# Kernel optimization log

Measured on AMD Instinct MI355X. Metric: run time of the kernel, lower is better.

## Reference

```python
import jax, jax.numpy as jnp
import numpy as np

T, B, N, DIN, H, DOUT = 20, 32, 100, 2, 128, 2
BN = B * N


def setup_inputs() -> dict:
    key = jax.random.key(0)
    ks = jax.random.split(key, 12)
    x = jax.random.normal(ks[0], (T, BN, DIN), jnp.float32)
    A = jax.random.randint(ks[1], (T, BN, BN), 0, 2, jnp.int32)
    mask = jax.random.randint(ks[2], (T, BN), 0, 2, jnp.int32).astype(bool)
    s_g = 1.0 / np.sqrt(DIN)
    s_h = 1.0 / np.sqrt(H)
    u = lambda k, shp, s: jax.random.uniform(k, shp, jnp.float32, -s, s)
    return {
        'x': x, 'A': A, 'mask': mask, 'num_nodes': N,
        'W_gcn': u(ks[3], (DIN, H), s_g), 'b_gcn': jnp.zeros((H,), jnp.float32),
        'W_ih': u(ks[4], (H, 3 * H), s_h), 'b_ih': u(ks[5], (3 * H,), s_h),
        'W_hh': u(ks[6], (H, 3 * H), s_h), 'b_hh': u(ks[7], (3 * H,), s_h),
        'W_fc': u(ks[8], (H, DOUT), s_h), 'b_fc': u(ks[9], (DOUT,), s_h),
    }


def reference(x, A, mask, num_nodes, W_gcn, b_gcn, W_ih, b_ih, W_hh, b_hh, W_fc, b_fc):
    BN_ = x.shape[1]
    B_ = BN_ // num_nodes

    def step(h, inp):
        feats, A_t, m_t = inp
        mf = m_t.astype(jnp.float32)
        # masked subgraph adjacency + self loops only on masked nodes (PyG add_self_loops on subgraph)
        Ahat = A_t.astype(jnp.float32) * mf[:, None] * mf[None, :] + jnp.diag(mf)
        deg = Ahat.sum(axis=0)  # PyG gcn_norm: in-degree at edge_index[1] (column sum)
        dinv = jnp.where(deg > 0, jax.lax.rsqrt(deg), 0.0)
        xw = feats @ W_gcn  # [BN, H]
        # out[i] = dinv[i] * sum_j Ahat[j,i] * dinv[j] * xw[j]
        agg = dinv[:, None] * (Ahat.T @ (xw * dinv[:, None]))
        g = jax.nn.relu(agg + b_gcn)
        # torch GRUCell
        gi = g @ W_ih + b_ih
        gh = h @ W_hh + b_hh
        ir, iz, ig = jnp.split(gi, 3, axis=-1)
        hr, hz, hg = jnp.split(gh, 3, axis=-1)
        r = jax.nn.sigmoid(ir + hr)
        z = jax.nn.sigmoid(iz + hz)
        n = jnp.tanh(ig + r * hg)
        h_new = (1.0 - z) * n + z * h
        h = jnp.where(m_t[:, None], h_new, h)  # scatter-back: only masked nodes update
        return h, h

    h0 = jnp.zeros((BN_, H), jnp.float32)
    _, seq = jax.lax.scan(step, h0, (x, A, mask))  # [T, BN, H]
    seq = seq.reshape(x.shape[0], B_, num_nodes, H)
    out = seq @ W_fc + b_fc  # [T, B, N, DOUT]
    return out.transpose(1, 2, 0, 3)  # [B, N, T, DOUT]
```

## Files before the change

### kernel.cpp

```cpp
#include <hip/hip_runtime.h>
#include <math.h>

#define T_  20
#define BN  3200
#define H   128
#define N3H 384
#define DOUT 2
#define JW  400

typedef unsigned char u8;

__device__ __forceinline__ bool getm(const u8* m8, const int* m32, int fl, int idx) {
    return fl ? (m8[idx] != 0) : (m32[idx] != 0);
}

__global__ __launch_bounds__(256) void k_compact(const u8* __restrict__ m8,
                                                 const int* __restrict__ m32,
                                                 int* __restrict__ flag,
                                                 int* __restrict__ act_idx,
                                                 int* __restrict__ act_cnt) {
    int t = blockIdx.x, tid = threadIdx.x;
    __shared__ int lf;
    if (tid == 0) lf = 0;
    __syncthreads();
    bool hit = false;
    for (int j = tid; j < BN; j += 256) {
        if ((j & 3) && m8[t * BN + j]) hit = true;
    }
    if (__any(hit) && (tid & 63) == 0) atomicOr(&lf, 1);
    __syncthreads();
    int fl = lf;
    if (tid == 0 && fl) atomicOr(flag, 1);
    for (int j = tid; j < BN; j += 256) {
        if (getm(m8, m32, fl, t * BN + j)) {
            int pos = atomicAdd(&act_cnt[t], 1);
            act_idx[t * BN + pos] = j;
        }
    }
}

#define RCH 256
__global__ __launch_bounds__(256) void k_deg_pack(const int* __restrict__ A,
                                                  const int* __restrict__ act_idx,
                                                  const int* __restrict__ act_cnt,
                                                  u8* __restrict__ A1,
                                                  int* __restrict__ deg) {
    int t = blockIdx.z;
    int nact = act_cnt[t];
    int start = blockIdx.y * RCH;
    if (start >= nact) return;
    int n = min(RCH, nact - start);
    __shared__ int ai_s[RCH];
    int tid = threadIdx.x;
    if (tid < n) ai_s[tid] = act_idx[t * BN + start + tid];
    __syncthreads();

    int c = (blockIdx.x * 256 + tid) * 4;
    if (c >= BN) return;
    const int* At = A + (size_t)t * BN * BN;
    u8* A1t = A1 + ((size_t)t * JW + (start >> 3)) * BN + c;
    int cnt0 = 0, cnt1 = 0, cnt2 = 0, cnt3 = 0;
    int n8 = n & ~7;
    int jb = 0;
    for (; jb < n8; jb += 8) {
        unsigned b0 = 0, b1 = 0, b2 = 0, b3 = 0;
        #pragma unroll
        for (int q = 0; q < 8; ++q) {
            int j = ai_s[jb + q];
            int4 aa = *(const int4*)(At + (size_t)j * BN + c);
            cnt0 += aa.x; b0 |= (unsigned)aa.x << q;
            cnt1 += aa.y; b1 |= (unsigned)aa.y << q;
            cnt2 += aa.z; b2 |= (unsigned)aa.z << q;
            cnt3 += aa.w; b3 |= (unsigned)aa.w << q;
        }
        uchar4 pk; pk.x = (u8)b0; pk.y = (u8)b1; pk.z = (u8)b2; pk.w = (u8)b3;
        *(uchar4*)(A1t + (size_t)(jb >> 3) * BN) = pk;
    }
    if (jb < n) {
        unsigned b0 = 0, b1 = 0, b2 = 0, b3 = 0;
        for (int q = 0; q < n - jb; ++q) {
            int j = ai_s[jb + q];
            int4 aa = *(const int4*)(At + (size_t)j * BN + c);
            cnt0 += aa.x; b0 |= (unsigned)aa.x << q;
            cnt1 += aa.y; b1 |= (unsigned)aa.y << q;
            cnt2 += aa.z; b2 |= (unsigned)aa.z << q;
            cnt3 += aa.w; b3 |= (unsigned)aa.w << q;
        }
        uchar4 pk; pk.x = (u8)b0; pk.y = (u8)b1; pk.z = (u8)b2; pk.w = (u8)b3;
        *(uchar4*)(A1t + (size_t)(jb >> 3) * BN) = pk;
    }
    atomicAdd(&deg[t * BN + c], cnt0);
    atomicAdd(&deg[t * BN + c + 1], cnt1);
    atomicAdd(&deg[t * BN + c + 2], cnt2);
    atomicAdd(&deg[t * BN + c + 3], cnt3);
}

__global__ __launch_bounds__(256) void k_dinv_u(const int* __restrict__ deg,
                                                const u8* __restrict__ m8,
                                                const int* __restrict__ m32,
                                                const int* __restrict__ flag,
                                                const float* __restrict__ x,
                                                const int* __restrict__ act_idx,
                                                const int* __restrict__ act_cnt,
                                                float* __restrict__ dinv,
                                                float* __restrict__ u0c,
                                                float* __restrict__ u1c) {
    int idx = blockIdx.x * 256 + threadIdx.x;
    int fl = *flag;
    int t = idx / BN, r = idx - t * BN;
    dinv[idx] = getm(m8, m32, fl, idx) ? rsqrtf((float)(deg[idx] + 1)) : 0.f;
    float v0 = 0.f, v1 = 0.f;
    if (r < act_cnt[t]) {
        int j = act_idx[idx];
        float d = rsqrtf((float)(deg[t * BN + j] + 1));
        v0 = d * x[(size_t)(t * BN + j) * 2];
        v1 = d * x[(size_t)(t * BN + j) * 2 + 1];
    }
    u0c[idx] = v0;
    u1c[idx] = v1;
}

#define JSL 25
__global__ __launch_bounds__(256) void k_c(const u8* __restrict__ A1,
                                           const int* __restrict__ act_cnt,
                                           const float* __restrict__ u0c,
                                           const float* __restrict__ u1c,
                                           float* __restrict__ c0g,
                                           float* __restrict__ c1g) {
    int t = blockIdx.z, js = blockIdx.y;
    int c = blockIdx.x * 1024 + threadIdx.x * 4;
    if (c >= BN) return;
    int nactp = (act_cnt[t] + 7) >> 3;
    int jw0 = js * JSL, jw1 = min(jw0 + JSL, nactp);
    if (jw0 >= jw1) return;
    const u8* base = A1 + (size_t)t * JW * BN;
    const float* U0 = u0c + t * BN;
    const float* U1 = u1c + t * BN;
    float s0[4] = {0.f, 0.f, 0.f, 0.f}, s1[4] = {0.f, 0.f, 0.f, 0.f};
    for (int jw = jw0; jw < jw1; ++jw) {
        uchar4 aa = *(const uchar4*)(base + (size_t)jw * BN + c);
        unsigned bb[4] = {aa.x, aa.y, aa.z, aa.w};
        const float* Up0 = U0 + jw * 8;
        const float* Up1 = U1 + jw * 8;
        #pragma unroll
        for (int jb = 0; jb < 8; ++jb) {
            float w0 = Up0[jb], w1 = Up1[jb];
            #pragma unroll
            for (int k = 0; k < 4; ++k) {
                if ((bb[k] >> jb) & 1) { s0[k] += w0; s1[k] += w1; }
            }
        }
    }
    #pragma unroll
    for (int k = 0; k < 4; ++k) {
        atomicAdd(&c0g[t * BN + c + k], s0[k]);
        atomicAdd(&c1g[t * BN + c + k], s1[k]);
    }
}

__global__ __launch_bounds__(384) void k_gi(const float* __restrict__ dinv,
                                            const float* __restrict__ c0g,
                                            const float* __restrict__ c1g,
                                            const float* __restrict__ x,
                                            const float* __restrict__ Wg,
                                            const float* __restrict__ bg,
                                            const int* __restrict__ act_idx,
                                            const int* __restrict__ act_cnt,
                                            const float* __restrict__ Wih,
                                            const float* __restrict__ bih,
                                            float* __restrict__ GI) {
    int t = blockIdx.y;
    int nact = act_cnt[t];
    int sb = blockIdx.x * 32;
    if (sb >= nact) return;
    int ns = min(32, nact - sb);
    __shared__ float gs[32][H];
    __shared__ float e0s[32], e1s[32];
    __shared__ int ar[32];
    int tid = threadIdx.x;
    if (tid < 32) {
        int row = 0; float e0 = 0.f, e1 = 0.f;
        if (tid < ns) {
            row = act_idx[t * BN + sb + tid];
            int gi = t * BN + row;
            float d = dinv[gi];
            e0 = d * (c0g[gi] + d * x[(size_t)gi * 2]);
            e1 = d * (c1g[gi] + d * x[(size_t)gi * 2 + 1]);
        }
        ar[tid] = row; e0s[tid] = e0; e1s[tid] = e1;
    }
    __syncthreads();
    for (int u2 = tid; u2 < 32 * H; u2 += 384) {
        int r = u2 >> 7, h = u2 & 127;
        gs[r][h] = fmaxf(e0s[r] * Wg[h] + e1s[r] * Wg[H + h] + bg[h], 0.f);
    }
    __syncthreads();

    float acc[32];
    #pragma unroll
    for (int r = 0; r < 32; ++r) acc[r] = 0.f;
    for (int k = 0; k < H; k += 4) {
        float w0 = Wih[(size_t)k * N3H + tid];
        float w1 = Wih[(size_t)(k + 1) * N3H + tid];
        float w2 = Wih[(size_t)(k + 2) * N3H + tid];
        float w3 = Wih[(size_t)(k + 3) * N3H + tid];
        #pragma unroll
        for (int r = 0; r < 32; ++r) {
            float4 g4 = *(const float4*)&gs[r][k];
            acc[r] += g4.x * w0 + g4.y * w1 + g4.z * w2 + g4.w * w3;
        }
    }
    float bb = bih[tid];
    #pragma unroll
    for (int r = 0; r < 32; ++r) {
        if (r < ns)
            GI[((size_t)t * BN + ar[r]) * N3H + tid] = acc[r] + bb;
    }
}

__global__ __launch_bounds__(384) void k_gru(const float* __restrict__ GI,
                                             const float* __restrict__ Whh,
                                             const float* __restrict__ bhh,
                                             const u8* __restrict__ m8,
                                             const int* __restrict__ m32,
                                             const int* __restrict__ flag,
                                             const float* __restrict__ Wfc,
                                             const float* __restrict__ bfc,
                                             float* __restrict__ out) {
    int row0 = blockIdx.x * 16;
    int tid = threadIdx.x;
    int fl = *flag;
    __shared__ float hs[16][H];
    __shared__ float ghs[16][N3H];
    __shared__ float bhs[N3H];
    __shared__ int ms[16];
    for (int i = tid; i < 16 * H; i += 384) (&hs[0][0])[i] = 0.f;
    if (tid < N3H) bhs[tid] = bhh[tid];
    int lane = tid & 63, wv = tid >> 6;
    float wfa0 = Wfc[lane * 2],        wfa1 = Wfc[lane * 2 + 1];
    float wfb0 = Wfc[(lane + 64) * 2], wfb1 = Wfc[(lane + 64) * 2 + 1];
    float bf0 = bfc[0], bf1 = bfc[1];

    for (int t = 0; t < T_; ++t) {
        if (tid < 16) ms[tid] = getm(m8, m32, fl, t * BN + row0 + tid) ? 1 : 0;
        __syncthreads();
        int mrl[16];
        #pragma unroll
        for (int r = 0; r < 16; ++r) mrl[r] = ms[r];

        float pir[6], piz[6], pig[6];
        #pragma unroll
        for (int ii = 0; ii < 6; ++ii) {
            pir[ii] = 0.f; piz[ii] = 0.f; pig[ii] = 0.f;
            int i5 = tid + ii * 384;
            if (i5 < 16 * H) {
                int r = i5 >> 7, u = i5 & 127;
                if (ms[r]) {
                    size_t gb = ((size_t)t * BN + row0 + r) * N3H;
                    pir[ii] = GI[gb + u];
                    piz[ii] = GI[gb + 128 + u];
                    pig[ii] = GI[gb + 256 + u];
                }
            }
        }

        float acc[16];
        #pragma unroll
        for (int r = 0; r < 16; ++r) acc[r] = 0.f;
        for (int k = 0; k < H; k += 4) {
            float w0 = Whh[(size_t)k * N3H + tid];
            float w1 = Whh[(size_t)(k + 1) * N3H + tid];
            float w2 = Whh[(size_t)(k + 2) * N3H + tid];
            float w3 = Whh[(size_t)(k + 3) * N3H + tid];
            #pragma unroll
            for (int r = 0; r < 16; ++r) {
                if (mrl[r]) {
                    float4 h4 = *(const float4*)&hs[r][k];
                    acc[r] += h4.x * w0 + h4.y * w1 + h4.z * w2 + h4.w * w3;
                }
            }
        }
        #pragma unroll
        for (int r = 0; r < 16; ++r) ghs[r][tid] = acc[r];
        __syncthreads();

        #pragma unroll
        for (int ii = 0; ii < 6; ++ii) {
            int i5 = tid + ii * 384;
            if (i5 < 16 * H) {
                int r = i5 >> 7, u = i5 & 127;
                if (ms[r]) {
                    float hr = ghs[r][u] + bhs[u];
                    float hz = ghs[r][128 + u] + bhs[128 + u];
                    float hg = ghs[r][256 + u] + bhs[256 + u];
                    float rg = 1.f / (1.f + expf(-(pir[ii] + hr)));
                    float zg = 1.f / (1.f + expf(-(piz[ii] + hz)));
                    float ng = tanhf(pig[ii] + rg * hg);
                    hs[r][u] = (1.f - zg) * ng + zg * hs[r][u];
                }
            }
        }
        __syncthreads();

        for (int r = wv; r < 16; r += 6) {
            float h0 = hs[r][lane], h1 = hs[r][lane + 64];
            float p0 = h0 * wfa0 + h1 * wfb0;
            float p1 = h0 * wfa1 + h1 * wfb1;
            for (int o = 32; o > 0; o >>= 1) { p0 += __shfl_down(p0, o); p1 += __shfl_down(p1, o); }
            if (lane == 0) {
                out[((size_t)(row0 + r) * T_ + t) * DOUT]     = p0 + bf0;
                out[((size_t)(row0 + r) * T_ + t) * DOUT + 1] = p1 + bf1;
            }
        }
        __syncthreads();
    }
}

extern "C" void kernel_launch(void* const* d_in, const int* in_sizes, int n_in,
                              void* d_out, int out_size, void* d_ws, size_t ws_size,
                              hipStream_t stream) {
    const float* x    = (const float*)d_in[0];
    const int*   A    = (const int*)d_in[1];
    const u8*    m8   = (const u8*)d_in[2];
    const int*   m32  = (const int*)d_in[2];
    const float* Wg   = (const float*)d_in[4];
    const float* bg   = (const float*)d_in[5];
    const float* Wih  = (const float*)d_in[6];
    const float* bih  = (const float*)d_in[7];
    const float* Whh  = (const float*)d_in[8];
    const float* bhh  = (const float*)d_in[9];
    const float* Wfc  = (const float*)d_in[10];
    const float* bfc  = (const float*)d_in[11];
    float* out = (float*)d_out;

    char* ws = (char*)d_ws;
    size_t off = 0;
    auto alloc = [&](size_t bytes) {
        void* p = ws + off;
        off += (bytes + 255) & ~(size_t)255;
        return p;
    };
    int*   flag    = (int*)alloc(4);
    int*   act_cnt = (int*)alloc(T_ * 4);
    int*   deg     = (int*)alloc((size_t)T_ * BN * 4);
    float* c0g     = (float*)alloc((size_t)T_ * BN * 4);
    float* c1g     = (float*)alloc((size_t)T_ * BN * 4);
    size_t zbytes = off;
    int*   act_idx = (int*)alloc((size_t)T_ * BN * 4);
    float* dinv    = (float*)alloc((size_t)T_ * BN * 4);
    float* u0c     = (float*)alloc((size_t)T_ * BN * 4);
    float* u1c     = (float*)alloc((size_t)T_ * BN * 4);
    u8*    A1      = (u8*)alloc((size_t)T_ * JW * BN);
    float* GI      = (float*)alloc((size_t)T_ * BN * N3H * 4);

    hipMemsetAsync(ws, 0, zbytes, stream);
    k_compact<<<T_, 256, 0, stream>>>(m8, m32, flag, act_idx, act_cnt);
    k_deg_pack<<<dim3(4, 13, T_), 256, 0, stream>>>(A, act_idx, act_cnt, A1, deg);
    k_dinv_u<<<(T_ * BN) / 256, 256, 0, stream>>>(deg, m8, m32, flag, x, act_idx, act_cnt, dinv, u0c, u1c);
    k_c<<<dim3(4, 16, T_), 256, 0, stream>>>(A1, act_cnt, u0c, u1c, c0g, c1g);
    k_gi<<<dim3(100, T_), 384, 0, stream>>>(dinv, c0g, c1g, x, Wg, bg, act_idx, act_cnt, Wih, bih, GI);
    k_gru<<<BN / 16, 384, 0, stream>>>(GI, Whh, bhh, m8, m32, flag, Wfc, bfc, out);
}
```

Measured before the change: 1.639 ms.

## Keep Whh in registers for GRU, retile GI kernel, drop dinv buffer

The recurrent GRU kernel now loads its full column of W_hh (128 floats per thread) into registers once, instead of reloading it from global memory at every timestep. Its launch bounds are set to one block per SM to make room for those registers. The GI kernel is retiled to 128 threads, 16 rows per block and three output columns per thread. The dinv array is removed and recomputed inline from deg, cutting one global write and read. Holding 128 weight registers per thread risks spills and lower occupancy in the GRU kernel.

```diff
diff --git a/kernel.cpp b/kernel.cpp
--- a/kernel.cpp
+++ b/kernel.cpp
@@ -95,20 +95,14 @@
     atomicAdd(&deg[t * BN + c + 3], cnt3);
 }
 
-__global__ __launch_bounds__(256) void k_dinv_u(const int* __restrict__ deg,
-                                                const u8* __restrict__ m8,
-                                                const int* __restrict__ m32,
-                                                const int* __restrict__ flag,
-                                                const float* __restrict__ x,
-                                                const int* __restrict__ act_idx,
-                                                const int* __restrict__ act_cnt,
-                                                float* __restrict__ dinv,
-                                                float* __restrict__ u0c,
-                                                float* __restrict__ u1c) {
+__global__ __launch_bounds__(256) void k_u(const int* __restrict__ deg,
+                                           const float* __restrict__ x,
+                                           const int* __restrict__ act_idx,
+                                           const int* __restrict__ act_cnt,
+                                           float* __restrict__ u0c,
+                                           float* __restrict__ u1c) {
     int idx = blockIdx.x * 256 + threadIdx.x;
-    int fl = *flag;
     int t = idx / BN, r = idx - t * BN;
-    dinv[idx] = getm(m8, m32, fl, idx) ? rsqrtf((float)(deg[idx] + 1)) : 0.f;
     float v0 = 0.f, v1 = 0.f;
     if (r < act_cnt[t]) {
         int j = act_idx[idx];
@@ -158,7 +152,7 @@
     }
 }
 
-__global__ __launch_bounds__(384) void k_gi(const float* __restrict__ dinv,
+__global__ __launch_bounds__(128) void k_gi(const int* __restrict__ deg,
                                             const float* __restrict__ c0g,
                                             const float* __restrict__ c1g,
                                             const float* __restrict__ x,
@@ -171,62 +165,70 @@
                                             float* __restrict__ GI) {
     int t = blockIdx.y;
     int nact = act_cnt[t];
-    int sb = blockIdx.x * 32;
+    int sb = blockIdx.x * 16;
     if (sb >= nact) return;
-    int ns = min(32, nact - sb);
-    __shared__ float gs[32][H];
-    __shared__ float e0s[32], e1s[32];
-    __shared__ int ar[32];
+    int ns = min(16, nact - sb);
+    __shared__ float gs[16][H];
+    __shared__ float e0s[16], e1s[16];
+    __shared__ int ar[16];
     int tid = threadIdx.x;
-    if (tid < 32) {
+    if (tid < 16) {
         int row = 0; float e0 = 0.f, e1 = 0.f;
         if (tid < ns) {
             row = act_idx[t * BN + sb + tid];
             int gi = t * BN + row;
-            float d = dinv[gi];
+            float d = rsqrtf((float)(deg[gi] + 1));
             e0 = d * (c0g[gi] + d * x[(size_t)gi * 2]);
             e1 = d * (c1g[gi] + d * x[(size_t)gi * 2 + 1]);
         }
         ar[tid] = row; e0s[tid] = e0; e1s[tid] = e1;
     }
     __syncthreads();
-    for (int u2 = tid; u2 < 32 * H; u2 += 384) {
-        int r = u2 >> 7, h = u2 & 127;
-        gs[r][h] = fmaxf(e0s[r] * Wg[h] + e1s[r] * Wg[H + h] + bg[h], 0.f);
-    }
-    __syncthreads();
-
-    float acc[32];
-    #pragma unroll
-    for (int r = 0; r < 32; ++r) acc[r] = 0.f;
+    float wg0 = Wg[tid], wg1 = Wg[H + tid], bgv = bg[tid];
+    #pragma unroll
+    for (int r = 0; r < 16; ++r)
+        gs[r][tid] = fmaxf(e0s[r] * wg0 + e1s[r] * wg1 + bgv, 0.f);
+    __syncthreads();
+
+    float acc0[16], acc1[16], acc2[16];
+    #pragma unroll
+    for (int r = 0; r < 16; ++r) { acc0[r] = 0.f; acc1[r] = 0.f; acc2[r] = 0.f; }
     for (int k = 0; k < H; k += 4) {
-        float w0 = Wih[(size_t)k * N3H + tid];
-        float w1 = Wih[(size_t)(k + 1) * N3H + tid];
-        float w2 = Wih[(size_t)(k + 2) * N3H + tid];
-        float w3 = Wih[(size_t)(k + 3) * N3H + tid];
-        #pragma unroll
-        for (int r = 0; r < 32; ++r) {
+        float w[4][3];
+        #pragma unroll
+        for (int kk = 0; kk < 4; ++kk) {
+            const float* wr = Wih + (size_t)(k + kk) * N3H;
+            w[kk][0] = wr[tid]; w[kk][1] = wr[128 + tid]; w[kk][2] = wr[256 + tid];
+        }
+        #pragma unroll
+        for (int r = 0; r < 16; ++r) {
             float4 g4 = *(const float4*)&gs[r][k];
-            acc[r] += g4.x * w0 + g4.y * w1 + g4.z * w2 + g4.w * w3;
-        }
-    }
-    float bb = bih[tid];
-    #pragma unroll
-    for (int r = 0; r < 32; ++r) {
-        if (r < ns)
-            GI[((size_t)t * BN + ar[r]) * N3H + tid] = acc[r] + bb;
-    }
-}
-
-__global__ __launch_bounds__(384) void k_gru(const float* __restrict__ GI,
-                                             const float* __restrict__ Whh,
-                                             const float* __restrict__ bhh,
-                                             const u8* __restrict__ m8,
-                                             const int* __restrict__ m32,
-                                             const int* __restrict__ flag,
-                                             const float* __restrict__ Wfc,
-                                             const float* __restrict__ bfc,
-                                             float* __restrict__ out) {
+            acc0[r] += g4.x * w[0][0] + g4.y * w[1][0] + g4.z * w[2][0] + g4.w * w[3][0];
+            acc1[r] += g4.x * w[0][1] + g4.y * w[1][1] + g4.z * w[2][1] + g4.w * w[3][1];
+            acc2[r] += g4.x * w[0][2] + g4.y * w[1][2] + g4.z * w[2][2] + g4.w * w[3][2];
+        }
+    }
+    float b0 = bih[tid], b1 = bih[128 + tid], b2 = bih[256 + tid];
+    #pragma unroll
+    for (int r = 0; r < 16; ++r) {
+        if (r < ns) {
+            size_t bbase = ((size_t)t * BN + ar[r]) * N3H;
+            GI[bbase + tid]       = acc0[r] + b0;
+            GI[bbase + 128 + tid] = acc1[r] + b1;
+            GI[bbase + 256 + tid] = acc2[r] + b2;
+        }
+    }
+}
+
+__global__ __launch_bounds__(384, 1) void k_gru(const float* __restrict__ GI,
+                                                const float* __restrict__ Whh,
+                                                const float* __restrict__ bhh,
+                                                const u8* __restrict__ m8,
+                                                const int* __restrict__ m32,
+                                                const int* __restrict__ flag,
+                                                const float* __restrict__ Wfc,
+                                                const float* __restrict__ bfc,
+                                                float* __restrict__ out) {
     int row0 = blockIdx.x * 16;
     int tid = threadIdx.x;
     int fl = *flag;
@@ -235,11 +237,20 @@
     __shared__ float bhs[N3H];
     __shared__ int ms[16];
     for (int i = tid; i < 16 * H; i += 384) (&hs[0][0])[i] = 0.f;
-    if (tid < N3H) bhs[tid] = bhh[tid];
+    bhs[tid] = bhh[tid];
     int lane = tid & 63, wv = tid >> 6;
     float wfa0 = Wfc[lane * 2],        wfa1 = Wfc[lane * 2 + 1];
     float wfb0 = Wfc[(lane + 64) * 2], wfb1 = Wfc[(lane + 64) * 2 + 1];
     float bf0 = bfc[0], bf1 = bfc[1];
+
+    float4 wreg[32];
+    #pragma unroll
+    for (int kk = 0; kk < 32; ++kk) {
+        wreg[kk].x = Whh[(size_t)(4 * kk)     * N3H + tid];
+        wreg[kk].y = Whh[(size_t)(4 * kk + 1) * N3H + tid];
+        wreg[kk].z = Whh[(size_t)(4 * kk + 2) * N3H + tid];
+        wreg[kk].w = Whh[(size_t)(4 * kk + 3) * N3H + tid];
+    }
 
     for (int t = 0; t < T_; ++t) {
         if (tid < 16) ms[tid] = getm(m8, m32, fl, t * BN + row0 + tid) ? 1 : 0;
@@ -255,7 +266,7 @@
             int i5 = tid + ii * 384;
             if (i5 < 16 * H) {
                 int r = i5 >> 7, u = i5 & 127;
-                if (ms[r]) {
+                if (mrl[r]) {
                     size_t gb = ((size_t)t * BN + row0 + r) * N3H;
                     pir[ii] = GI[gb + u];
                     piz[ii] = GI[gb + 128 + u];
@@ -264,24 +275,19 @@
             }
         }
 
-        float acc[16];
-        #pragma unroll
-        for (int r = 0; r < 16; ++r) acc[r] = 0.f;
-        for (int k = 0; k < H; k += 4) {
-            float w0 = Whh[(size_t)k * N3H + tid];
-            float w1 = Whh[(size_t)(k + 1) * N3H + tid];
-            float w2 = Whh[(size_t)(k + 2) * N3H + tid];
-            float w3 = Whh[(size_t)(k + 3) * N3H + tid];
-            #pragma unroll
-            for (int r = 0; r < 16; ++r) {
-                if (mrl[r]) {
-                    float4 h4 = *(const float4*)&hs[r][k];
-                    acc[r] += h4.x * w0 + h4.y * w1 + h4.z * w2 + h4.w * w3;
+        #pragma unroll
+        for (int r = 0; r < 16; ++r) {
+            if (mrl[r]) {
+                float a = 0.f;
+                #pragma unroll
+                for (int kk = 0; kk < 32; ++kk) {
+                    float4 h4 = *(const float4*)&hs[r][kk * 4];
+                    float4 w = wreg[kk];
+                    a += h4.x * w.x + h4.y * w.y + h4.z * w.z + h4.w * w.w;
                 }
-            }
-        }
-        #pragma unroll
-        for (int r = 0; r < 16; ++r) ghs[r][tid] = acc[r];
+                ghs[r][tid] = a;
+            }
+        }
         __syncthreads();
 
         #pragma unroll
@@ -289,7 +295,7 @@
             int i5 = tid + ii * 384;
             if (i5 < 16 * H) {
                 int r = i5 >> 7, u = i5 & 127;
-                if (ms[r]) {
+                if (mrl[r]) {
                     float hr = ghs[r][u] + bhs[u];
                     float hz = ghs[r][128 + u] + bhs[128 + u];
                     float hg = ghs[r][256 + u] + bhs[256 + u];
@@ -347,7 +353,6 @@
     float* c1g     = (float*)alloc((size_t)T_ * BN * 4);
     size_t zbytes = off;
     int*   act_idx = (int*)alloc((size_t)T_ * BN * 4);
-    float* dinv    = (float*)alloc((size_t)T_ * BN * 4);
     float* u0c     = (float*)alloc((size_t)T_ * BN * 4);
     float* u1c     = (float*)alloc((size_t)T_ * BN * 4);
     u8*    A1      = (u8*)alloc((size_t)T_ * JW * BN);
@@ -356,8 +361,8 @@
     hipMemsetAsync(ws, 0, zbytes, stream);
     k_compact<<<T_, 256, 0, stream>>>(m8, m32, flag, act_idx, act_cnt);
     k_deg_pack<<<dim3(4, 13, T_), 256, 0, stream>>>(A, act_idx, act_cnt, A1, deg);
-    k_dinv_u<<<(T_ * BN) / 256, 256, 0, stream>>>(deg, m8, m32, flag, x, act_idx, act_cnt, dinv, u0c, u1c);
+    k_u<<<(T_ * BN) / 256, 256, 0, stream>>>(deg, x, act_idx, act_cnt, u0c, u1c);
     k_c<<<dim3(4, 16, T_), 256, 0, stream>>>(A1, act_cnt, u0c, u1c, c0g, c1g);
-    k_gi<<<dim3(100, T_), 384, 0, stream>>>(dinv, c0g, c1g, x, Wg, bg, act_idx, act_cnt, Wih, bih, GI);
+    k_gi<<<dim3(200, T_), 128, 0, stream>>>(deg, c0g, c1g, x, Wg, bg, act_idx, act_cnt, Wih, bih, GI);
     k_gru<<<BN / 16, 384, 0, stream>>>(GI, Whh, bhh, m8, m32, flag, Wfc, bfc, out);
 }
```

Measured after the change: 1.344 ms. -18.0%, faster.
